# Kernel tuning notes

Measured on AMD Instinct MI355X. Metric: run time of the kernel, lower is better.

The kernel has to match this reference:

```python
import jax, jax.numpy as jnp
import numpy as np
import math

THETA = 10000.0

def apply_rope(x, start_pos=0):
    # x: [B, H, S, D], rotate-half RoPE
    B, H, S, D = x.shape
    pos = jnp.arange(start_pos, start_pos + S, dtype=jnp.float32)
    inv_freq = 1.0 / (THETA ** (jnp.arange(0, D, 2, dtype=jnp.float32) / D))  # [D/2]
    ang = pos[:, None] * inv_freq[None, :]  # [S, D/2]
    cos, sin = jnp.cos(ang), jnp.sin(ang)
    x1, x2 = jnp.split(x, 2, axis=-1)
    return jnp.concatenate([x1 * cos - x2 * sin, x1 * sin + x2 * cos], axis=-1)


def setup_inputs() -> dict:
    key = jax.random.key(0)
    ks = jax.random.split(key, 9)
    B, S, E, H, D = 2, 2048, 2048, 16, 128
    s = 0.02
    return {
        "x": jax.random.normal(ks[0], (B, S, E), jnp.float32),
        "W_q": jax.random.normal(ks[1], (E, H * D), jnp.float32) * s,
        "b_q": jnp.zeros((H * D,), jnp.float32),
        "W_k": jax.random.normal(ks[2], (E, D), jnp.float32) * s,
        "b_k": jnp.zeros((D,), jnp.float32),
        "W_v": jax.random.normal(ks[3], (E, D), jnp.float32) * s,
        "b_v": jnp.zeros((D,), jnp.float32),
        "W_o": jax.random.normal(ks[4], (H * D, E), jnp.float32) * s,
        "b_o": jnp.zeros((E,), jnp.float32),
    }


def reference(x, W_q, b_q, W_k, b_k, W_v, b_v, W_o, b_o):
    B, S, E = x.shape
    D = W_k.shape[1]
    H = W_q.shape[1] // D
    # projections (weights stored [in, out])
    q = (x @ W_q + b_q).reshape(B, S, H, D).transpose(0, 2, 1, 3)   # [B,H,S,D]
    k = (x @ W_k + b_k).reshape(B, S, 1, D).transpose(0, 2, 1, 3)   # [B,1,S,D]
    v = (x @ W_v + b_v).reshape(B, S, 1, D).transpose(0, 2, 1, 3)   # [B,1,S,D]
    # RoPE (cache is None -> start_pos = 0)
    q = apply_rope(q, 0)
    k = apply_rope(k, 0)
    # shared-KV attention: k head dim broadcasts over H q heads
    scores = jnp.einsum("bhqd,bokd->bhqk", q, k) / math.sqrt(D)     # [B,H,S,S]
    causal = jnp.tril(jnp.ones((S, S), dtype=bool))
    scores = jnp.where(causal, scores, -jnp.inf)
    attn = jax.nn.softmax(scores, axis=-1)
    out = jnp.einsum("bhqk,bokd->bhqd", attn, v)                    # [B,H,S,D]
    out = out.transpose(0, 2, 1, 3).reshape(B, S, H * D)
    out = out @ W_o + b_o                                           # dropout is identity in eval
    return out
```

## Files before the change

kernel.cpp:

```cpp
#include <hip/hip_runtime.h>
#include <stdint.h>

typedef __bf16 bf16x8 __attribute__((ext_vector_type(8)));
typedef float  f32x4  __attribute__((ext_vector_type(4)));
typedef short  s16x8  __attribute__((ext_vector_type(8)));

__device__ inline unsigned short f2b(float f) {
  unsigned int u = __builtin_bit_cast(unsigned int, f);
  u += 0x7FFFu + ((u >> 16) & 1u);
  return (unsigned short)(u >> 16);
}
__device__ inline float b2f(unsigned short h) {
  unsigned int u = ((unsigned int)h) << 16;
  return __builtin_bit_cast(float, u);
}
__device__ inline unsigned int pk2(float a, float b) {
  return (unsigned int)f2b(a) | ((unsigned int)f2b(b) << 16);
}
__device__ inline void gload_lds16(const void* g, void* l) {
  __builtin_amdgcn_global_load_lds(
      (const __attribute__((address_space(1))) unsigned int*)g,
      (__attribute__((address_space(3))) unsigned int*)l, 16, 0, 0);
}

__global__ void k_cvt_bf16(const float* __restrict__ in, unsigned short* __restrict__ out, int n4) {
  int i = blockIdx.x * blockDim.x + threadIdx.x;
  if (i < n4) {
    float4 v = ((const float4*)in)[i];
    ushort4 o;
    o.x = f2b(v.x); o.y = f2b(v.y); o.z = f2b(v.z); o.w = f2b(v.w);
    ((ushort4*)out)[i] = o;
  }
}

__global__ void k_transpose(const float* __restrict__ A, int nA,
                            const float* __restrict__ Bsrc, int nB,
                            const float* __restrict__ Csrc,
                            unsigned short* __restrict__ dst, int K) {
  __shared__ float tile[32][33];
  int n0 = blockIdx.x * 32;
  int k0 = blockIdx.y * 32;
  const float* src; int ldn, noff;
  if (n0 < nA)            { src = A;    ldn = nA; noff = n0; }
  else if (n0 < nA + nB)  { src = Bsrc; ldn = nB; noff = n0 - nA; }
  else                    { src = Csrc; ldn = nB; noff = n0 - nA - nB; }
  int tx = threadIdx.x & 31, ty = threadIdx.x >> 5;
  for (int yy = ty; yy < 32; yy += 8)
    tile[yy][tx] = src[(size_t)(k0 + yy) * ldn + noff + tx];
  __syncthreads();
  for (int yy = ty; yy < 32; yy += 8)
    dst[(size_t)(n0 + yy) * K + k0 + tx] = f2b(tile[tx][yy]);
}

__global__ void k_bias_concat(const float* __restrict__ bq, const float* __restrict__ bk,
                              const float* __restrict__ bv, float* __restrict__ dst) {
  int i = blockIdx.x * 256 + threadIdx.x;
  if (i < 2304) dst[i] = (i < 2048) ? bq[i] : (i < 2176 ? bk[i - 2048] : bv[i - 2176]);
}

template<int OUT_BF16>
__global__ __launch_bounds__(256)
void k_gemm_bt(const unsigned short* __restrict__ A, const unsigned short* __restrict__ Bt,
               const float* __restrict__ bias, void* __restrict__ Cout,
               int M, int N, int K) {
  __shared__ unsigned short As[128][40];
  __shared__ unsigned short Bs[128][40];
  const int tid  = threadIdx.x;
  const int lane = tid & 63, wid = tid >> 6;
  const int lr = lane & 15, lk = lane >> 4;
  const int wr = wid >> 1,  wc = wid & 1;
  const int mb = blockIdx.y * 128, nb = blockIdx.x * 128;
  const int srow = tid >> 2, scol = (tid & 3) * 8;
  const size_t Abase = (size_t)(mb + srow) * K + scol;
  const size_t Bbase = (size_t)(nb + srow) * K + scol;

  f32x4 acc[4][4];
  #pragma unroll
  for (int i = 0; i < 4; ++i)
    #pragma unroll
    for (int j = 0; j < 4; ++j) acc[i][j] = (f32x4){0.f, 0.f, 0.f, 0.f};

  const int kt_num = K >> 5;
  s16x8 av0 = *(const s16x8*)(A  + Abase);
  s16x8 av1 = *(const s16x8*)(A  + Abase + 64 * (size_t)K);
  s16x8 bv0 = *(const s16x8*)(Bt + Bbase);
  s16x8 bv1 = *(const s16x8*)(Bt + Bbase + 64 * (size_t)K);

  for (int kt = 0; kt < kt_num; ++kt) {
    __syncthreads();
    *(s16x8*)&As[srow][scol]      = av0;
    *(s16x8*)&As[srow + 64][scol] = av1;
    *(s16x8*)&Bs[srow][scol]      = bv0;
    *(s16x8*)&Bs[srow + 64][scol] = bv1;
    __syncthreads();
    if (kt + 1 < kt_num) {
      size_t off = (size_t)(kt + 1) * 32;
      av0 = *(const s16x8*)(A  + Abase + off);
      av1 = *(const s16x8*)(A  + Abase + 64 * (size_t)K + off);
      bv0 = *(const s16x8*)(Bt + Bbase + off);
      bv1 = *(const s16x8*)(Bt + Bbase + 64 * (size_t)K + off);
    }
    bf16x8 af[4], bfv[4];
    #pragma unroll
    for (int m = 0; m < 4; ++m) af[m]  = *(const bf16x8*)&As[wr * 64 + m * 16 + lr][lk * 8];
    #pragma unroll
    for (int n = 0; n < 4; ++n) bfv[n] = *(const bf16x8*)&Bs[wc * 64 + n * 16 + lr][lk * 8];
    #pragma unroll
    for (int m = 0; m < 4; ++m)
      #pragma unroll
      for (int n = 0; n < 4; ++n)
        acc[m][n] = __builtin_amdgcn_mfma_f32_16x16x32_bf16(af[m], bfv[n], acc[m][n], 0, 0, 0);
  }

  const int r0 = mb + wr * 64, c0 = nb + wc * 64;
  #pragma unroll
  for (int m = 0; m < 4; ++m) {
    #pragma unroll
    for (int n = 0; n < 4; ++n) {
      int col = c0 + n * 16 + lr;
      float bb = bias[col];
      #pragma unroll
      for (int r = 0; r < 4; ++r) {
        int row = r0 + m * 16 + lk * 4 + r;
        float v = acc[m][n][r] + bb;
        if (OUT_BF16) ((unsigned short*)Cout)[(size_t)row * N + col] = f2b(v);
        else          ((float*)Cout)[(size_t)row * N + col] = v;
      }
    }
  }
}

__global__ void k_rope(const unsigned short* __restrict__ qkv,
                       unsigned short* __restrict__ qr,
                       unsigned short* __restrict__ kr,
                       int S, int H) {
  int R = blockIdx.x * 4 + (threadIdx.x >> 6);
  int lane = threadIdx.x & 63;
  int per_b = S * (H + 1);
  int b = R / per_b;
  int rem = R - b * per_b;
  int s = rem / (H + 1);
  int j = rem - s * (H + 1);
  const unsigned short* src = qkv + (size_t)(b * S + s) * 2304 + (j < H ? j * 128 : 2048);
  float x1 = b2f(src[lane]);
  float x2 = b2f(src[lane + 64]);
  float invf = expf(-(float)lane * (9.210340371976184f / 64.0f));
  float ang = (float)s * invf;
  float c = cosf(ang), sn = sinf(ang);
  float o1 = x1 * c - x2 * sn;
  float o2 = x1 * sn + x2 * c;
  unsigned short* dst;
  if (j < H) dst = qr + ((size_t)(b * H + j) * S + s) * 128;
  else       dst = kr + ((size_t)(b * S) + s) * 128;
  dst[lane]      = f2b(o1);
  dst[lane + 64] = f2b(o2);
}

__global__ void k_vtrans(const unsigned short* __restrict__ qkv,
                         unsigned short* __restrict__ vt, int S) {
  __shared__ unsigned short tile[32][33];
  int b = blockIdx.z;
  int s0 = blockIdx.x * 32, d0 = blockIdx.y * 32;
  int tx = threadIdx.x & 31, ty = threadIdx.x >> 5;
  for (int yy = ty; yy < 32; yy += 8)
    tile[yy][tx] = qkv[(size_t)(b * S + s0 + yy) * 2304 + 2176 + d0 + tx];
  __syncthreads();
  for (int yy = ty; yy < 32; yy += 8)
    vt[((size_t)b * 128 + d0 + yy) * S + s0 + tx] = tile[tx][yy];
}

__global__ __launch_bounds__(256)
void k_attn(const unsigned short* __restrict__ qr,
            const unsigned short* __restrict__ kr,
            const unsigned short* __restrict__ vt,
            unsigned short* __restrict__ attn_out,
            int S, int H) {
  const int b = blockIdx.z, h = blockIdx.y;
  const int tid = threadIdx.x, wid = tid >> 6, lane = tid & 63;
  const int lr = lane & 15, lk = lane >> 4;

  __shared__ unsigned short Kt[2][64 * 128];
  __shared__ unsigned short Vt[2][128 * 64];
  __shared__ unsigned short P_all[4][16][72];
  unsigned short (*P)[72] = P_all[wid];

  const char* kbyte = (const char*)(kr + (size_t)b * S * 128);
  const char* vbyte = (const char*)(vt + (size_t)b * 128 * S);
  const size_t vrow_bytes = (size_t)S * 2;

  const int krow0 = tid >> 4;
  const int kcb   = (tid & 15) << 4;
  const int vd0   = tid >> 3;
  const int vcb   = (tid & 7) << 4;
  const int lds_woff = (wid * 1024) >> 1;

  const int ksw = (lr & 7) << 4;

  const int ntiles = gridDim.x * 2;
  const float scale = 0.08838834764831845f;

  #pragma unroll 1
  for (int half = 0; half < 2; ++half) {
    const int qt  = (half == 0) ? blockIdx.x : (ntiles - 1 - blockIdx.x);
    const int qb0 = qt * 64;
    const int qw  = qb0 + wid * 16;

    const unsigned short* qptr = qr + ((size_t)(b * H + h) * S + (qw + lr)) * 128;
    bf16x8 aq[4];
    #pragma unroll
    for (int kk = 0; kk < 4; ++kk) aq[kk] = *(const bf16x8*)(qptr + kk * 32 + lk * 8);

    f32x4 accO[8];
    #pragma unroll
    for (int t = 0; t < 8; ++t) accO[t] = (f32x4){0.f, 0.f, 0.f, 0.f};
    float lsum = 0.f;

    auto stage = [&](int buf, int kb) {
      const char* kg = kbyte + (size_t)kb * 256;
      #pragma unroll
      for (int r = 0; r < 4; ++r) {
        int row = krow0 + r * 16;
        const char* src = kg + row * 256 + (kcb ^ ((row & 7) << 4));
        gload_lds16(src, (void*)(&Kt[buf][0] + lds_woff + r * 2048));
      }
      const char* vg = vbyte + (size_t)kb * 2;
      #pragma unroll
      for (int r = 0; r < 4; ++r) {
        int d = vd0 + r * 32;
        const char* src = vg + (size_t)d * vrow_bytes + (vcb ^ ((d & 7) << 4));
        gload_lds16(src, (void*)(&Vt[buf][0] + lds_woff + r * 2048));
      }
    };

    int cur = 0;
    stage(0, 0);
    __syncthreads();

    #pragma unroll 1
    for (int kb = 0; kb <= qb0; kb += 64) {
      if (kb + 64 <= qb0) stage(cur ^ 1, kb + 64);
      const bool diag = (kb == qb0);
      const unsigned short* Kc = &Kt[cur][0];
      const unsigned short* Vc = &Vt[cur][0];

      bf16x8 kf[4][4];
      #pragma unroll
      for (int m = 0; m < 4; ++m) {
        const char* kl = (const char*)(Kc + (m * 16 + lr) * 128);
        #pragma unroll
        for (int kk = 0; kk < 4; ++kk)
          kf[m][kk] = *(const bf16x8*)(kl + ((kk * 64 + lk * 16) ^ ksw));
      }
      f32x4 s4[4];
      #pragma unroll
      for (int m = 0; m < 4; ++m) s4[m] = (f32x4){0.f, 0.f, 0.f, 0.f};
      #pragma unroll
      for (int kk = 0; kk < 4; ++kk)
        #pragma unroll
        for (int m = 0; m < 4; ++m)
          s4[m] = __builtin_amdgcn_mfma_f32_16x16x32_bf16(kf[m][kk], aq[kk], s4[m], 0, 0, 0);

      #pragma unroll
      for (int m = 0; m < 4; ++m) {
        float p[4];
        #pragma unroll
        for (int r = 0; r < 4; ++r) {
          float v = __expf(s4[m][r] * scale);
          if (diag && (m * 16 + lk * 4 + r) > (wid * 16 + lr)) v = 0.f;
          p[r] = v;
          lsum += v;
        }
        uint2 w;
        w.x = pk2(p[0], p[1]);
        w.y = pk2(p[2], p[3]);
        *(uint2*)&P[lr][m * 16 + lk * 4] = w;
      }

      #pragma unroll
      for (int ks = 0; ks < 2; ++ks) {
        bf16x8 pa = *(const bf16x8*)&P[lr][ks * 32 + lk * 8];
        #pragma unroll
        for (int t = 0; t < 8; ++t) {
          const char* vl = (const char*)(Vc + (t * 16 + lr) * 64);
          bf16x8 bv = *(const bf16x8*)(vl + ((ks * 64 + lk * 16) ^ ksw));
          accO[t] = __builtin_amdgcn_mfma_f32_16x16x32_bf16(pa, bv, accO[t], 0, 0, 0);
        }
      }
      __syncthreads();
      cur ^= 1;
    }

    lsum += __shfl_xor(lsum, 16);
    lsum += __shfl_xor(lsum, 32);
    float rl[4];
    #pragma unroll
    for (int r = 0; r < 4; ++r) rl[r] = 1.0f / __shfl(lsum, lk * 4 + r);
    #pragma unroll
    for (int t = 0; t < 8; ++t) {
      #pragma unroll
      for (int r = 0; r < 4; ++r) {
        int srow = qw + lk * 4 + r;
        float o = accO[t][r] * rl[r];
        attn_out[((size_t)(b * S) + srow) * 2048 + h * 128 + t * 16 + lr] = f2b(o);
      }
    }
  }
}

extern "C" void kernel_launch(void* const* d_in, const int* in_sizes, int n_in,
                              void* d_out, int out_size, void* d_ws, size_t ws_size,
                              hipStream_t stream) {
  const float* x  = (const float*)d_in[0];
  const float* Wq = (const float*)d_in[1];
  const float* bq = (const float*)d_in[2];
  const float* Wk = (const float*)d_in[3];
  const float* bk = (const float*)d_in[4];
  const float* Wv = (const float*)d_in[5];
  const float* bv = (const float*)d_in[6];
  const float* Wo = (const float*)d_in[7];
  const float* bo = (const float*)d_in[8];

  const int B = 2, S = 2048, E = 2048, H = 16, D = 128;
  const int M = B * S;
  const int Nqkv = H * D + 2 * D;

  char* w = (char*)d_ws;
  unsigned short* xb    = (unsigned short*)w;
  unsigned short* WqkvT = (unsigned short*)(w + 16777216);
  unsigned short* qkv   = (unsigned short*)(w + 16777216 + 9437184);
  unsigned short* qr    = (unsigned short*)(w + 16777216 + 9437184 + 18874368);
  unsigned short* kr    = qr + (size_t)B * H * S * D;
  unsigned short* vtb   = kr + (size_t)B * S * D;
  float*          cbias = (float*)(vtb + (size_t)B * S * D);
  unsigned short* attn_out = xb;
  unsigned short* WoT      = WqkvT;

  k_cvt_bf16<<<dim3((M * E / 4) / 256), 256, 0, stream>>>(x, xb, M * E / 4);
  k_transpose<<<dim3(Nqkv / 32, E / 32), 256, 0, stream>>>(Wq, H * D, Wk, D, Wv, WqkvT, E);
  k_bias_concat<<<dim3(9), 256, 0, stream>>>(bq, bk, bv, cbias);
  k_gemm_bt<1><<<dim3(Nqkv / 128, M / 128), 256, 0, stream>>>(xb, WqkvT, cbias, (void*)qkv, M, Nqkv, E);
  k_rope<<<dim3(B * S * (H + 1) / 4), 256, 0, stream>>>(qkv, qr, kr, S, H);
  k_vtrans<<<dim3(S / 32, D / 32, B), 256, 0, stream>>>(qkv, vtb, S);
  k_transpose<<<dim3(E / 32, (H * D) / 32), 256, 0, stream>>>(Wo, E, nullptr, 0, nullptr, WoT, H * D);
  k_attn<<<dim3(S / 128, H, B), 256, 0, stream>>>(qr, kr, vtb, attn_out, S, H);
  k_gemm_bt<0><<<dim3(E / 128, M / 128), 256, 0, stream>>>(attn_out, WoT, bo, (void*)d_out, M, E, H * D);
}
```

Baseline: 216.5 us.

## Double-buffer GEMM via direct global-to-LDS loads and tune attention inner loop

The GEMM now stages A and B tiles straight into double-buffered LDS with global_load_lds and needs one barrier per k-step instead of two register round trips. This is meant to overlap the next tile's load with the current tile's MFMAs. The attention kernel raises wave priority around its MFMA blocks and packs to bf16 with hardware conversion instead of manual rounding. The 1/sqrt(D) scale is folded into Q during RoPE, which takes one multiply per score out of the attention loop. The unpadded LDS layout may cause bank conflicts, and applying the scale before bf16 rounding slightly changes numerics.

```diff
diff --git a/kernel.cpp b/kernel.cpp
--- a/kernel.cpp
+++ b/kernel.cpp
@@ -2,6 +2,7 @@
 #include <stdint.h>
 
 typedef __bf16 bf16x8 __attribute__((ext_vector_type(8)));
+typedef __bf16 bf16x2 __attribute__((ext_vector_type(2)));
 typedef float  f32x4  __attribute__((ext_vector_type(4)));
 typedef short  s16x8  __attribute__((ext_vector_type(8)));
 
@@ -14,8 +15,11 @@
   unsigned int u = ((unsigned int)h) << 16;
   return __builtin_bit_cast(float, u);
 }
-__device__ inline unsigned int pk2(float a, float b) {
-  return (unsigned int)f2b(a) | ((unsigned int)f2b(b) << 16);
+__device__ inline unsigned int pkcvt(float a, float b) {
+  bf16x2 t;
+  t[0] = (__bf16)a;
+  t[1] = (__bf16)b;
+  return __builtin_bit_cast(unsigned int, t);
 }
 __device__ inline void gload_lds16(const void* g, void* l) {
   __builtin_amdgcn_global_load_lds(
@@ -60,19 +64,21 @@
 
 template<int OUT_BF16>
 __global__ __launch_bounds__(256)
-void k_gemm_bt(const unsigned short* __restrict__ A, const unsigned short* __restrict__ Bt,
-               const float* __restrict__ bias, void* __restrict__ Cout,
-               int M, int N, int K) {
-  __shared__ unsigned short As[128][40];
-  __shared__ unsigned short Bs[128][40];
+void k_gemm_lds(const unsigned short* __restrict__ A, const unsigned short* __restrict__ Bt,
+                const float* __restrict__ bias, void* __restrict__ Cout,
+                int M, int N, int K) {
+  __shared__ unsigned short As[2][4096];
+  __shared__ unsigned short Bs[2][4096];
   const int tid  = threadIdx.x;
   const int lane = tid & 63, wid = tid >> 6;
   const int lr = lane & 15, lk = lane >> 4;
   const int wr = wid >> 1,  wc = wid & 1;
   const int mb = blockIdx.y * 128, nb = blockIdx.x * 128;
-  const int srow = tid >> 2, scol = (tid & 3) * 8;
-  const size_t Abase = (size_t)(mb + srow) * K + scol;
-  const size_t Bbase = (size_t)(nb + srow) * K + scol;
+
+  const int srow = tid >> 2, scb = (tid & 3) * 8;
+  const size_t gA = (size_t)(mb + srow) * K + scb;
+  const size_t gB = (size_t)(nb + srow) * K + scb;
+  const int ldso = wid * 512;
 
   f32x4 acc[4][4];
   #pragma unroll
@@ -80,36 +86,36 @@
     #pragma unroll
     for (int j = 0; j < 4; ++j) acc[i][j] = (f32x4){0.f, 0.f, 0.f, 0.f};
 
-  const int kt_num = K >> 5;
-  s16x8 av0 = *(const s16x8*)(A  + Abase);
-  s16x8 av1 = *(const s16x8*)(A  + Abase + 64 * (size_t)K);
-  s16x8 bv0 = *(const s16x8*)(Bt + Bbase);
-  s16x8 bv1 = *(const s16x8*)(Bt + Bbase + 64 * (size_t)K);
-
-  for (int kt = 0; kt < kt_num; ++kt) {
-    __syncthreads();
-    *(s16x8*)&As[srow][scol]      = av0;
-    *(s16x8*)&As[srow + 64][scol] = av1;
-    *(s16x8*)&Bs[srow][scol]      = bv0;
-    *(s16x8*)&Bs[srow + 64][scol] = bv1;
-    __syncthreads();
-    if (kt + 1 < kt_num) {
-      size_t off = (size_t)(kt + 1) * 32;
-      av0 = *(const s16x8*)(A  + Abase + off);
-      av1 = *(const s16x8*)(A  + Abase + 64 * (size_t)K + off);
-      bv0 = *(const s16x8*)(Bt + Bbase + off);
-      bv1 = *(const s16x8*)(Bt + Bbase + 64 * (size_t)K + off);
-    }
+  auto stage = [&](int buf, int kt) {
+    const size_t ko = (size_t)kt * 32;
+    gload_lds16(A  + gA + ko,            &As[buf][ldso]);
+    gload_lds16(A  + gA + 64 * (size_t)K + ko, &As[buf][2048 + ldso]);
+    gload_lds16(Bt + gB + ko,            &Bs[buf][ldso]);
+    gload_lds16(Bt + gB + 64 * (size_t)K + ko, &Bs[buf][2048 + ldso]);
+  };
+
+  const int ktn = K >> 5;
+  stage(0, 0);
+  __syncthreads();
+
+  int cur = 0;
+  #pragma unroll 1
+  for (int kt = 0; kt < ktn; ++kt) {
+    if (kt + 1 < ktn) stage(cur ^ 1, kt + 1);
     bf16x8 af[4], bfv[4];
     #pragma unroll
-    for (int m = 0; m < 4; ++m) af[m]  = *(const bf16x8*)&As[wr * 64 + m * 16 + lr][lk * 8];
-    #pragma unroll
-    for (int n = 0; n < 4; ++n) bfv[n] = *(const bf16x8*)&Bs[wc * 64 + n * 16 + lr][lk * 8];
+    for (int m = 0; m < 4; ++m)
+      af[m]  = *(const bf16x8*)&As[cur][(wr * 64 + m * 16 + lr) * 32 + lk * 8];
+    #pragma unroll
+    for (int n = 0; n < 4; ++n)
+      bfv[n] = *(const bf16x8*)&Bs[cur][(wc * 64 + n * 16 + lr) * 32 + lk * 8];
     #pragma unroll
     for (int m = 0; m < 4; ++m)
       #pragma unroll
       for (int n = 0; n < 4; ++n)
         acc[m][n] = __builtin_amdgcn_mfma_f32_16x16x32_bf16(af[m], bfv[n], acc[m][n], 0, 0, 0);
+    __syncthreads();
+    cur ^= 1;
   }
 
   const int r0 = mb + wr * 64, c0 = nb + wc * 64;
@@ -150,8 +156,13 @@
   float o1 = x1 * c - x2 * sn;
   float o2 = x1 * sn + x2 * c;
   unsigned short* dst;
-  if (j < H) dst = qr + ((size_t)(b * H + j) * S + s) * 128;
-  else       dst = kr + ((size_t)(b * S) + s) * 128;
+  if (j < H) {
+    const float scale = 0.08838834764831845f;
+    o1 *= scale; o2 *= scale;
+    dst = qr + ((size_t)(b * H + j) * S + s) * 128;
+  } else {
+    dst = kr + ((size_t)(b * S) + s) * 128;
+  }
   dst[lane]      = f2b(o1);
   dst[lane + 64] = f2b(o2);
 }
@@ -197,7 +208,6 @@
   const int ksw = (lr & 7) << 4;
 
   const int ntiles = gridDim.x * 2;
-  const float scale = 0.08838834764831845f;
 
   #pragma unroll 1
   for (int half = 0; half < 2; ++half) {
@@ -254,37 +264,41 @@
       f32x4 s4[4];
       #pragma unroll
       for (int m = 0; m < 4; ++m) s4[m] = (f32x4){0.f, 0.f, 0.f, 0.f};
+      __builtin_amdgcn_s_setprio(1);
       #pragma unroll
       for (int kk = 0; kk < 4; ++kk)
         #pragma unroll
         for (int m = 0; m < 4; ++m)
           s4[m] = __builtin_amdgcn_mfma_f32_16x16x32_bf16(kf[m][kk], aq[kk], s4[m], 0, 0, 0);
+      __builtin_amdgcn_s_setprio(0);
 
       #pragma unroll
       for (int m = 0; m < 4; ++m) {
         float p[4];
         #pragma unroll
         for (int r = 0; r < 4; ++r) {
-          float v = __expf(s4[m][r] * scale);
+          float v = __expf(s4[m][r]);
           if (diag && (m * 16 + lk * 4 + r) > (wid * 16 + lr)) v = 0.f;
           p[r] = v;
           lsum += v;
         }
         uint2 w;
-        w.x = pk2(p[0], p[1]);
-        w.y = pk2(p[2], p[3]);
+        w.x = pkcvt(p[0], p[1]);
+        w.y = pkcvt(p[2], p[3]);
         *(uint2*)&P[lr][m * 16 + lk * 4] = w;
       }
 
       #pragma unroll
       for (int ks = 0; ks < 2; ++ks) {
         bf16x8 pa = *(const bf16x8*)&P[lr][ks * 32 + lk * 8];
+        __builtin_amdgcn_s_setprio(1);
         #pragma unroll
         for (int t = 0; t < 8; ++t) {
           const char* vl = (const char*)(Vc + (t * 16 + lr) * 64);
           bf16x8 bv = *(const bf16x8*)(vl + ((ks * 64 + lk * 16) ^ ksw));
           accO[t] = __builtin_amdgcn_mfma_f32_16x16x32_bf16(pa, bv, accO[t], 0, 0, 0);
         }
+        __builtin_amdgcn_s_setprio(0);
       }
       __syncthreads();
       cur ^= 1;
@@ -338,10 +352,10 @@
   k_cvt_bf16<<<dim3((M * E / 4) / 256), 256, 0, stream>>>(x, xb, M * E / 4);
   k_transpose<<<dim3(Nqkv / 32, E / 32), 256, 0, stream>>>(Wq, H * D, Wk, D, Wv, WqkvT, E);
   k_bias_concat<<<dim3(9), 256, 0, stream>>>(bq, bk, bv, cbias);
-  k_gemm_bt<1><<<dim3(Nqkv / 128, M / 128), 256, 0, stream>>>(xb, WqkvT, cbias, (void*)qkv, M, Nqkv, E);
+  k_gemm_lds<1><<<dim3(Nqkv / 128, M / 128), 256, 0, stream>>>(xb, WqkvT, cbias, (void*)qkv, M, Nqkv, E);
   k_rope<<<dim3(B * S * (H + 1) / 4), 256, 0, stream>>>(qkv, qr, kr, S, H);
   k_vtrans<<<dim3(S / 32, D / 32, B), 256, 0, stream>>>(qkv, vtb, S);
   k_transpose<<<dim3(E / 32, (H * D) / 32), 256, 0, stream>>>(Wo, E, nullptr, 0, nullptr, WoT, H * D);
   k_attn<<<dim3(S / 128, H, B), 256, 0, stream>>>(qr, kr, vtb, attn_out, S, H);
-  k_gemm_bt<0><<<dim3(E / 128, M / 128), 256, 0, stream>>>(attn_out, WoT, bo, (void*)d_out, M, E, H * D);
-}
+  k_gemm_lds<0><<<dim3(E / 128, M / 128), 256, 0, stream>>>(attn_out, WoT, bo, (void*)d_out, M, E, H * D);
+}
```

Measured after the change: 213.2 us. About the same (-1.5%).
